# Performance work log

Hardware: AMD Instinct MI355X
Metric: run time of the kernel (lower is better)

The kernel has to match this reference:

```python
import jax, jax.numpy as jnp
import numpy as np

E = 8        # num_experts
K = 2        # num_experts_per_tok
H = 2048     # hidden_size
I = 1024     # intermediate_size (c_fc outputs 2*I for swiglu)
T = 4096     # tokens (batch*seq flattened)
STD = 0.02


def setup_inputs() -> dict:
    key = jax.random.key(0)
    k1, k2, k3, k4 = jax.random.split(key, 4)
    x = jax.random.normal(k1, (T, H), dtype=jnp.float32)
    router_w = jax.random.normal(k2, (E, H), dtype=jnp.float32) * STD   # nn.Linear(H->E, bias=False)
    w1 = jax.random.normal(k3, (E, 2 * I, H), dtype=jnp.float32) * STD  # c_fc.weight (E, out, in)
    w2 = jax.random.normal(k4, (E, H, I), dtype=jnp.float32) * STD      # c_proj.weight (E, out, in)
    return {"x": x, "router_w": router_w, "w1": w1, "w2": w2}


def reference(x, router_w, w1, w2):
    # Router: logits -> fp32 softmax -> top-k gates (no renorm), as in scattermoe-style MoE
    logits = x @ router_w.T                                   # (T, E)
    probs = jax.nn.softmax(logits.astype(jnp.float32), axis=-1)
    gates, expert_idx = jax.lax.top_k(probs, K)               # (T, K)

    # Grouped expert GEMMs, expressed densely over the small fixed expert axis.
    up = jnp.einsum('th,efh->etf', x, w1)                     # (E, T, 2I)  c_fc
    g = up[..., ::2]                                          # interleaved GLU gate
    u = up[..., 1::2]
    h = u * jax.nn.silu(g)                                    # swiglu, (E, T, I)
    y = jnp.einsum('eti,ehi->eth', h, w2)                     # (E, T, H)  c_proj

    # Scatter-combine: pick each token's top-k expert outputs, weight by gates.
    t = jnp.arange(T)[:, None]                                # (T, 1)
    sel = y[expert_idx, t]                                    # (T, K, H)
    out = jnp.sum(gates[..., None].astype(x.dtype) * sel, axis=1)  # (T, H)
    return out
```

## Files before the change

kernel.cpp:

```cpp
#include <hip/hip_runtime.h>
#include <hip/hip_bf16.h>
#include <stdint.h>

#define T_TOK 4096
#define H_DIM 2048
#define I_DIM 1024
#define E_NUM 8

using bf16x8  = __attribute__((ext_vector_type(8))) __bf16;
using f32x4   = __attribute__((ext_vector_type(4))) float;
using ushort8 = __attribute__((ext_vector_type(8))) unsigned short;

__device__ __forceinline__ unsigned short f2bf(float f) {
  unsigned int u = __float_as_uint(f);
  u += 0x7fffu + ((u >> 16) & 1u);
  return (unsigned short)(u >> 16);
}

__global__ void k_router(const float* __restrict__ x, const float* __restrict__ rw,
                         float* __restrict__ gates, int* __restrict__ idxs,
                         unsigned int* __restrict__ counts, unsigned short* __restrict__ xb) {
  int t = blockIdx.x;
  int lane = threadIdx.x;
  float acc[E_NUM];
#pragma unroll
  for (int e = 0; e < E_NUM; e++) acc[e] = 0.f;
  const float* xrow = x + (size_t)t * H_DIM;
  for (int h = lane; h < H_DIM; h += 64) {
    float xv = xrow[h];
    xb[(size_t)t * H_DIM + h] = f2bf(xv);
#pragma unroll
    for (int e = 0; e < E_NUM; e++) acc[e] += xv * rw[e * H_DIM + h];
  }
#pragma unroll
  for (int e = 0; e < E_NUM; e++) {
#pragma unroll
    for (int off = 32; off >= 1; off >>= 1) acc[e] += __shfl_xor(acc[e], off, 64);
  }
  if (lane == 0) {
    float mx = acc[0];
#pragma unroll
    for (int e = 1; e < E_NUM; e++) mx = fmaxf(mx, acc[e]);
    float p[E_NUM], s = 0.f;
#pragma unroll
    for (int e = 0; e < E_NUM; e++) { p[e] = __expf(acc[e] - mx); s += p[e]; }
    float inv = 1.f / s;
#pragma unroll
    for (int e = 0; e < E_NUM; e++) p[e] *= inv;
    int i1 = 0, i2 = 0; float m1 = -1.f, m2 = -1.f;
#pragma unroll
    for (int e = 0; e < E_NUM; e++) {
      float v = p[e];
      if (v > m1)      { m2 = m1; i2 = i1; m1 = v; i1 = e; }
      else if (v > m2) { m2 = v; i2 = e; }
    }
    gates[t * 2 + 0] = m1; gates[t * 2 + 1] = m2;
    idxs[t * 2 + 0] = i1;  idxs[t * 2 + 1] = i2;
    atomicAdd(&counts[i1], 1u);
    atomicAdd(&counts[i2], 1u);
  }
}

__global__ void k_offsets(const unsigned int* __restrict__ counts,
                          unsigned int* __restrict__ off, unsigned int* __restrict__ cursor) {
  if (threadIdx.x == 0 && blockIdx.x == 0) {
    unsigned int o = 0;
    for (int e = 0; e < E_NUM; e++) { off[e] = o; cursor[e] = o; o += counts[e]; }
  }
}

__global__ void k_scatter(const float* __restrict__ gates, const int* __restrict__ idxs,
                          unsigned int* __restrict__ cursor,
                          int* __restrict__ rowlist, float* __restrict__ rowgate) {
  int t = blockIdx.x * blockDim.x + threadIdx.x;
  if (t >= T_TOK) return;
#pragma unroll
  for (int k = 0; k < 2; k++) {
    int e = idxs[t * 2 + k];
    unsigned int pos = atomicAdd(&cursor[e], 1u);
    rowlist[pos] = t;
    rowgate[pos] = gates[t * 2 + k];
  }
}

__launch_bounds__(256, 2)
__global__ void k_gemm1(const unsigned short* __restrict__ xb, const float* __restrict__ w1,
                        const unsigned int* __restrict__ off, const unsigned int* __restrict__ counts,
                        const int* __restrict__ rowlist, unsigned short* __restrict__ hc) {
  int e = blockIdx.z;
  unsigned int cnt = counts[e];
  unsigned int rb = blockIdx.y;
  if (rb * 128u >= cnt) return;
  unsigned int o = off[e];
  int i0 = blockIdx.x * 64;

  __shared__ unsigned short a_lds[128 * 40];
  __shared__ unsigned short bg_lds[64 * 40];
  __shared__ unsigned short bu_lds[64 * 40];

  int tid = threadIdx.x;
  int lane = tid & 63;
  int wave = tid >> 6;
  int wr = wave >> 1;
  int wc = wave & 1;

  const float* w1e = w1 + (size_t)e * (2 * I_DIM) * H_DIM;

  f32x4 accg[4][2], accu[4][2];
#pragma unroll
  for (int m = 0; m < 4; m++)
#pragma unroll
    for (int n = 0; n < 2; n++) {
      accg[m][n] = f32x4{0.f, 0.f, 0.f, 0.f};
      accu[m][n] = f32x4{0.f, 0.f, 0.f, 0.f};
    }

  const unsigned short* asrc[2];
#pragma unroll
  for (int it = 0; it < 2; it++) {
    int flat = it * 256 + tid;
    int row = flat >> 2;
    unsigned int pos = rb * 128u + (unsigned int)row;
    unsigned int gp = o + (pos < cnt ? pos : cnt - 1u);
    int tok = rowlist[gp];
    asrc[it] = xb + (size_t)tok * H_DIM;
  }

  for (int k0 = 0; k0 < H_DIM; k0 += 32) {
    __syncthreads();
#pragma unroll
    for (int it = 0; it < 2; it++) {
      int flat = it * 256 + tid;
      int row = flat >> 2, q = flat & 3;
      ushort8 v = *reinterpret_cast<const ushort8*>(asrc[it] + k0 + q * 8);
      *reinterpret_cast<ushort8*>(&a_lds[row * 40 + q * 8]) = v;
    }
#pragma unroll
    for (int it = 0; it < 2; it++) {
      int flat = it * 256 + tid;
      int fl = flat >> 2, q = flat & 3;
      const float* src = w1e + (size_t)(2 * i0 + fl) * H_DIM + k0 + q * 8;
      float4 v0 = *reinterpret_cast<const float4*>(src);
      float4 v1 = *reinterpret_cast<const float4*>(src + 4);
      ushort8 b;
      b[0] = f2bf(v0.x); b[1] = f2bf(v0.y); b[2] = f2bf(v0.z); b[3] = f2bf(v0.w);
      b[4] = f2bf(v1.x); b[5] = f2bf(v1.y); b[6] = f2bf(v1.z); b[7] = f2bf(v1.w);
      unsigned short* dst = (fl & 1) ? bu_lds : bg_lds;
      *reinterpret_cast<ushort8*>(&dst[(fl >> 1) * 40 + q * 8]) = b;
    }
    __syncthreads();

    bf16x8 af[4], bgf[2], buf_[2];
#pragma unroll
    for (int m = 0; m < 4; m++) {
      int row = wr * 64 + m * 16 + (lane & 15);
      af[m] = *reinterpret_cast<const bf16x8*>(&a_lds[row * 40 + (lane >> 4) * 8]);
    }
#pragma unroll
    for (int n = 0; n < 2; n++) {
      int c = wc * 32 + n * 16 + (lane & 15);
      bgf[n]  = *reinterpret_cast<const bf16x8*>(&bg_lds[c * 40 + (lane >> 4) * 8]);
      buf_[n] = *reinterpret_cast<const bf16x8*>(&bu_lds[c * 40 + (lane >> 4) * 8]);
    }
#pragma unroll
    for (int m = 0; m < 4; m++)
#pragma unroll
      for (int n = 0; n < 2; n++) {
        accg[m][n] = __builtin_amdgcn_mfma_f32_16x16x32_bf16(af[m], bgf[n],  accg[m][n], 0, 0, 0);
        accu[m][n] = __builtin_amdgcn_mfma_f32_16x16x32_bf16(af[m], buf_[n], accu[m][n], 0, 0, 0);
      }
  }

#pragma unroll
  for (int m = 0; m < 4; m++)
#pragma unroll
    for (int n = 0; n < 2; n++)
#pragma unroll
      for (int r = 0; r < 4; r++) {
        unsigned int grow = rb * 128u + wr * 64 + m * 16 + (lane >> 4) * 4 + r;
        if (grow < cnt) {
          float g = accg[m][n][r], u = accu[m][n][r];
          float h = u * g / (1.f + __expf(-g));
          int ic = i0 + wc * 32 + n * 16 + (lane & 15);
          hc[(size_t)(o + grow) * I_DIM + ic] = f2bf(h);
        }
      }
}

__launch_bounds__(256, 2)
__global__ void k_gemm2(const unsigned short* __restrict__ hc, const float* __restrict__ w2,
                        const unsigned int* __restrict__ off, const unsigned int* __restrict__ counts,
                        const int* __restrict__ rowlist, const float* __restrict__ rowgate,
                        float* __restrict__ out) {
  int e = blockIdx.z;
  unsigned int cnt = counts[e];
  unsigned int rb = blockIdx.y;
  if (rb * 128u >= cnt) return;
  unsigned int o = off[e];
  int h0 = blockIdx.x * 128;

  __shared__ unsigned short a_lds[128 * 40];
  __shared__ unsigned short b_lds[128 * 40];

  int tid = threadIdx.x;
  int lane = tid & 63;
  int wave = tid >> 6;
  int wr = wave >> 1;
  int wc = wave & 1;

  const float* w2e = w2 + (size_t)e * H_DIM * I_DIM;

  f32x4 acc[4][4];
#pragma unroll
  for (int m = 0; m < 4; m++)
#pragma unroll
    for (int n = 0; n < 4; n++) acc[m][n] = f32x4{0.f, 0.f, 0.f, 0.f};

  const unsigned short* asrc[2];
#pragma unroll
  for (int it = 0; it < 2; it++) {
    int flat = it * 256 + tid;
    int row = flat >> 2;
    unsigned int pos = rb * 128u + (unsigned int)row;
    unsigned int gp = o + (pos < cnt ? pos : cnt - 1u);
    asrc[it] = hc + (size_t)gp * I_DIM;
  }

  for (int k0 = 0; k0 < I_DIM; k0 += 32) {
    __syncthreads();
#pragma unroll
    for (int it = 0; it < 2; it++) {
      int flat = it * 256 + tid;
      int row = flat >> 2, q = flat & 3;
      ushort8 v = *reinterpret_cast<const ushort8*>(asrc[it] + k0 + q * 8);
      *reinterpret_cast<ushort8*>(&a_lds[row * 40 + q * 8]) = v;
    }
#pragma unroll
    for (int it = 0; it < 2; it++) {
      int flat = it * 256 + tid;
      int fl = flat >> 2, q = flat & 3;
      const float* src = w2e + (size_t)(h0 + fl) * I_DIM + k0 + q * 8;
      float4 v0 = *reinterpret_cast<const float4*>(src);
      float4 v1 = *reinterpret_cast<const float4*>(src + 4);
      ushort8 b;
      b[0] = f2bf(v0.x); b[1] = f2bf(v0.y); b[2] = f2bf(v0.z); b[3] = f2bf(v0.w);
      b[4] = f2bf(v1.x); b[5] = f2bf(v1.y); b[6] = f2bf(v1.z); b[7] = f2bf(v1.w);
      *reinterpret_cast<ushort8*>(&b_lds[fl * 40 + q * 8]) = b;
    }
    __syncthreads();

    bf16x8 af[4], bf[4];
#pragma unroll
    for (int m = 0; m < 4; m++) {
      int row = wr * 64 + m * 16 + (lane & 15);
      af[m] = *reinterpret_cast<const bf16x8*>(&a_lds[row * 40 + (lane >> 4) * 8]);
    }
#pragma unroll
    for (int n = 0; n < 4; n++) {
      int c = wc * 64 + n * 16 + (lane & 15);
      bf[n] = *reinterpret_cast<const bf16x8*>(&b_lds[c * 40 + (lane >> 4) * 8]);
    }
#pragma unroll
    for (int m = 0; m < 4; m++)
#pragma unroll
      for (int n = 0; n < 4; n++)
        acc[m][n] = __builtin_amdgcn_mfma_f32_16x16x32_bf16(af[m], bf[n], acc[m][n], 0, 0, 0);
  }

#pragma unroll
  for (int m = 0; m < 4; m++)
#pragma unroll
    for (int r = 0; r < 4; r++) {
      unsigned int grow = rb * 128u + wr * 64 + m * 16 + (lane >> 4) * 4 + r;
      if (grow < cnt) {
        int tok = rowlist[o + grow];
        float gate = rowgate[o + grow];
        float* orow = out + (size_t)tok * H_DIM + h0 + wc * 64;
#pragma unroll
        for (int n = 0; n < 4; n++) {
          atomicAdd(&orow[n * 16 + (lane & 15)], gate * acc[m][n][r]);
        }
      }
    }
}

extern "C" void kernel_launch(void* const* d_in, const int* in_sizes, int n_in,
                              void* d_out, int out_size, void* d_ws, size_t ws_size,
                              hipStream_t stream) {
  const float* x  = (const float*)d_in[0];
  const float* rw = (const float*)d_in[1];
  const float* w1 = (const float*)d_in[2];
  const float* w2 = (const float*)d_in[3];
  float* out = (float*)d_out;

  char* ws = (char*)d_ws;
  unsigned int* counts = (unsigned int*)(ws + 0);
  unsigned int* cursor = (unsigned int*)(ws + 64);
  unsigned int* off    = (unsigned int*)(ws + 128);
  float* gates   = (float*)(ws + 4096);
  int*   idxs    = (int*)(ws + 4096 + 32768);
  int*   rowlist = (int*)(ws + 4096 + 65536);
  float* rowgate = (float*)(ws + 4096 + 98304);
  unsigned short* xb = (unsigned short*)(ws + (1u << 20));
  unsigned short* hc = (unsigned short*)(ws + (18u << 20));

  hipMemsetAsync(ws, 0, 256, stream);
  hipMemsetAsync(d_out, 0, (size_t)out_size * sizeof(float), stream);

  k_router<<<T_TOK, 64, 0, stream>>>(x, rw, gates, idxs, counts, xb);
  k_offsets<<<1, 64, 0, stream>>>(counts, off, cursor);
  k_scatter<<<T_TOK / 256, 256, 0, stream>>>(gates, idxs, cursor, rowlist, rowgate);
  k_gemm1<<<dim3(I_DIM / 64, T_TOK / 128, E_NUM), 256, 0, stream>>>(xb, w1, off, counts, rowlist, hc);
  k_gemm2<<<dim3(H_DIM / 128, T_TOK / 128, E_NUM), 256, 0, stream>>>(hc, w2, off, counts, rowlist, rowgate, out);
}
```

Baseline: 635.6 us.

## Pre-convert expert weights to bf16 and stream tiles via global_load_lds

Adds kernels that convert w1 (de-interleaved into separate gate and up planes) and w2 to bf16 once per call. The two GEMM kernels then load A and B tiles directly from global memory into LDS with global_load_lds, with no per-tile fp32 loads, conversion or register staging. The LDS row pitch drops from 40 to 32 elements, which may bring back bank conflicts, and launch bounds are raised to 3 blocks per CU. The cost is an extra pass over the fp32 weights plus a bf16 write and re-read, in exchange for halving weight traffic inside the GEMMs and removing repeated conversion work across row blocks.

```diff
diff --git a/kernel.cpp b/kernel.cpp
--- a/kernel.cpp
+++ b/kernel.cpp
@@ -15,6 +15,40 @@
   unsigned int u = __float_as_uint(f);
   u += 0x7fffu + ((u >> 16) & 1u);
   return (unsigned short)(u >> 16);
+}
+
+__device__ __forceinline__ void gload16(const unsigned short* g, unsigned short* l) {
+  __builtin_amdgcn_global_load_lds(
+      (const __attribute__((address_space(1))) unsigned int*)(g),
+      (__attribute__((address_space(3))) unsigned int*)(l), 16, 0, 0);
+}
+
+__global__ void k_cvt_w1(const float* __restrict__ w1, unsigned short* __restrict__ w1b) {
+  size_t idx = (size_t)blockIdx.x * 256 + threadIdx.x;
+  size_t d = idx * 8;
+  int h = (int)(d & (size_t)(H_DIM - 1));
+  size_t rem = d >> 11;
+  int i = (int)(rem & (size_t)(I_DIM - 1));
+  size_t rem2 = rem >> 10;
+  int gu = (int)(rem2 & 1);
+  int e = (int)(rem2 >> 1);
+  const float* src = w1 + (((size_t)e * 2 * I_DIM + 2 * i + gu) * H_DIM + h);
+  float4 v0 = *reinterpret_cast<const float4*>(src);
+  float4 v1 = *reinterpret_cast<const float4*>(src + 4);
+  ushort8 b;
+  b[0] = f2bf(v0.x); b[1] = f2bf(v0.y); b[2] = f2bf(v0.z); b[3] = f2bf(v0.w);
+  b[4] = f2bf(v1.x); b[5] = f2bf(v1.y); b[6] = f2bf(v1.z); b[7] = f2bf(v1.w);
+  *reinterpret_cast<ushort8*>(w1b + d) = b;
+}
+
+__global__ void k_cvt_w2(const float* __restrict__ w2, unsigned short* __restrict__ w2b) {
+  size_t d = ((size_t)blockIdx.x * 256 + threadIdx.x) * 8;
+  float4 v0 = *reinterpret_cast<const float4*>(w2 + d);
+  float4 v1 = *reinterpret_cast<const float4*>(w2 + d + 4);
+  ushort8 b;
+  b[0] = f2bf(v0.x); b[1] = f2bf(v0.y); b[2] = f2bf(v0.z); b[3] = f2bf(v0.w);
+  b[4] = f2bf(v1.x); b[5] = f2bf(v1.y); b[6] = f2bf(v1.z); b[7] = f2bf(v1.w);
+  *reinterpret_cast<ushort8*>(w2b + d) = b;
 }
 
 __global__ void k_router(const float* __restrict__ x, const float* __restrict__ rw,
@@ -83,8 +117,8 @@
   }
 }
 
-__launch_bounds__(256, 2)
-__global__ void k_gemm1(const unsigned short* __restrict__ xb, const float* __restrict__ w1,
+__launch_bounds__(256, 3)
+__global__ void k_gemm1(const unsigned short* __restrict__ xb, const unsigned short* __restrict__ w1b,
                         const unsigned int* __restrict__ off, const unsigned int* __restrict__ counts,
                         const int* __restrict__ rowlist, unsigned short* __restrict__ hc) {
   int e = blockIdx.z;
@@ -94,17 +128,31 @@
   unsigned int o = off[e];
   int i0 = blockIdx.x * 64;
 
-  __shared__ unsigned short a_lds[128 * 40];
-  __shared__ unsigned short bg_lds[64 * 40];
-  __shared__ unsigned short bu_lds[64 * 40];
-
-  int tid = threadIdx.x;
-  int lane = tid & 63;
-  int wave = tid >> 6;
-  int wr = wave >> 1;
-  int wc = wave & 1;
-
-  const float* w1e = w1 + (size_t)e * (2 * I_DIM) * H_DIM;
+  __shared__ unsigned short a_lds[128 * 32];
+  __shared__ unsigned short bg_lds[64 * 32];
+  __shared__ unsigned short bu_lds[64 * 32];
+
+  int tid = threadIdx.x, lane = tid & 63, wave = tid >> 6;
+  int wr = wave >> 1, wc = wave & 1;
+
+  const unsigned short* aptr[2];
+  unsigned short* alds[2];
+#pragma unroll
+  for (int it = 0; it < 2; it++) {
+    int flat = wave * 128 + it * 64 + lane;
+    int row = flat >> 2, colq = flat & 3;
+    unsigned int pos = rb * 128u + (unsigned int)row;
+    unsigned int gp = o + (pos < cnt ? pos : cnt - 1u);
+    int tok = rowlist[gp];
+    aptr[it] = xb + (size_t)tok * H_DIM + colq * 8;
+    alds[it] = &a_lds[(wave * 2 + it) * 512];
+  }
+  int flatB = wave * 64 + lane;
+  int brow = flatB >> 2, bcolq = flatB & 3;
+  const unsigned short* bptr_g = w1b + ((size_t)(e * 2 + 0) * I_DIM + i0 + brow) * H_DIM + bcolq * 8;
+  const unsigned short* bptr_u = w1b + ((size_t)(e * 2 + 1) * I_DIM + i0 + brow) * H_DIM + bcolq * 8;
+  unsigned short* blds_g = &bg_lds[wave * 512];
+  unsigned short* blds_u = &bu_lds[wave * 512];
 
   f32x4 accg[4][2], accu[4][2];
 #pragma unroll
@@ -115,52 +163,25 @@
       accu[m][n] = f32x4{0.f, 0.f, 0.f, 0.f};
     }
 
-  const unsigned short* asrc[2];
-#pragma unroll
-  for (int it = 0; it < 2; it++) {
-    int flat = it * 256 + tid;
-    int row = flat >> 2;
-    unsigned int pos = rb * 128u + (unsigned int)row;
-    unsigned int gp = o + (pos < cnt ? pos : cnt - 1u);
-    int tok = rowlist[gp];
-    asrc[it] = xb + (size_t)tok * H_DIM;
-  }
-
   for (int k0 = 0; k0 < H_DIM; k0 += 32) {
     __syncthreads();
-#pragma unroll
-    for (int it = 0; it < 2; it++) {
-      int flat = it * 256 + tid;
-      int row = flat >> 2, q = flat & 3;
-      ushort8 v = *reinterpret_cast<const ushort8*>(asrc[it] + k0 + q * 8);
-      *reinterpret_cast<ushort8*>(&a_lds[row * 40 + q * 8]) = v;
-    }
-#pragma unroll
-    for (int it = 0; it < 2; it++) {
-      int flat = it * 256 + tid;
-      int fl = flat >> 2, q = flat & 3;
-      const float* src = w1e + (size_t)(2 * i0 + fl) * H_DIM + k0 + q * 8;
-      float4 v0 = *reinterpret_cast<const float4*>(src);
-      float4 v1 = *reinterpret_cast<const float4*>(src + 4);
-      ushort8 b;
-      b[0] = f2bf(v0.x); b[1] = f2bf(v0.y); b[2] = f2bf(v0.z); b[3] = f2bf(v0.w);
-      b[4] = f2bf(v1.x); b[5] = f2bf(v1.y); b[6] = f2bf(v1.z); b[7] = f2bf(v1.w);
-      unsigned short* dst = (fl & 1) ? bu_lds : bg_lds;
-      *reinterpret_cast<ushort8*>(&dst[(fl >> 1) * 40 + q * 8]) = b;
-    }
+    gload16(aptr[0] + k0, alds[0]);
+    gload16(aptr[1] + k0, alds[1]);
+    gload16(bptr_g + k0, blds_g);
+    gload16(bptr_u + k0, blds_u);
     __syncthreads();
 
     bf16x8 af[4], bgf[2], buf_[2];
 #pragma unroll
     for (int m = 0; m < 4; m++) {
       int row = wr * 64 + m * 16 + (lane & 15);
-      af[m] = *reinterpret_cast<const bf16x8*>(&a_lds[row * 40 + (lane >> 4) * 8]);
+      af[m] = *reinterpret_cast<const bf16x8*>(&a_lds[row * 32 + (lane >> 4) * 8]);
     }
 #pragma unroll
     for (int n = 0; n < 2; n++) {
       int c = wc * 32 + n * 16 + (lane & 15);
-      bgf[n]  = *reinterpret_cast<const bf16x8*>(&bg_lds[c * 40 + (lane >> 4) * 8]);
-      buf_[n] = *reinterpret_cast<const bf16x8*>(&bu_lds[c * 40 + (lane >> 4) * 8]);
+      bgf[n]  = *reinterpret_cast<const bf16x8*>(&bg_lds[c * 32 + (lane >> 4) * 8]);
+      buf_[n] = *reinterpret_cast<const bf16x8*>(&bu_lds[c * 32 + (lane >> 4) * 8]);
     }
 #pragma unroll
     for (int m = 0; m < 4; m++)
@@ -187,8 +208,8 @@
       }
 }
 
-__launch_bounds__(256, 2)
-__global__ void k_gemm2(const unsigned short* __restrict__ hc, const float* __restrict__ w2,
+__launch_bounds__(256, 3)
+__global__ void k_gemm2(const unsigned short* __restrict__ hc, const unsigned short* __restrict__ w2b,
                         const unsigned int* __restrict__ off, const unsigned int* __restrict__ counts,
                         const int* __restrict__ rowlist, const float* __restrict__ rowgate,
                         float* __restrict__ out) {
@@ -199,66 +220,51 @@
   unsigned int o = off[e];
   int h0 = blockIdx.x * 128;
 
-  __shared__ unsigned short a_lds[128 * 40];
-  __shared__ unsigned short b_lds[128 * 40];
-
-  int tid = threadIdx.x;
-  int lane = tid & 63;
-  int wave = tid >> 6;
-  int wr = wave >> 1;
-  int wc = wave & 1;
-
-  const float* w2e = w2 + (size_t)e * H_DIM * I_DIM;
+  __shared__ unsigned short a_lds[128 * 32];
+  __shared__ unsigned short b_lds[128 * 32];
+
+  int tid = threadIdx.x, lane = tid & 63, wave = tid >> 6;
+  int wr = wave >> 1, wc = wave & 1;
+
+  const unsigned short* aptr[2];
+  const unsigned short* bptr[2];
+  unsigned short *alds[2], *blds[2];
+#pragma unroll
+  for (int it = 0; it < 2; it++) {
+    int flat = wave * 128 + it * 64 + lane;
+    int row = flat >> 2, colq = flat & 3;
+    unsigned int pos = rb * 128u + (unsigned int)row;
+    unsigned int posc = (pos < cnt ? pos : cnt - 1u);
+    aptr[it] = hc + (size_t)(o + posc) * I_DIM + colq * 8;
+    bptr[it] = w2b + ((size_t)e * H_DIM + h0 + row) * I_DIM + colq * 8;
+    alds[it] = &a_lds[(wave * 2 + it) * 512];
+    blds[it] = &b_lds[(wave * 2 + it) * 512];
+  }
 
   f32x4 acc[4][4];
 #pragma unroll
   for (int m = 0; m < 4; m++)
 #pragma unroll
     for (int n = 0; n < 4; n++) acc[m][n] = f32x4{0.f, 0.f, 0.f, 0.f};
-
-  const unsigned short* asrc[2];
-#pragma unroll
-  for (int it = 0; it < 2; it++) {
-    int flat = it * 256 + tid;
-    int row = flat >> 2;
-    unsigned int pos = rb * 128u + (unsigned int)row;
-    unsigned int gp = o + (pos < cnt ? pos : cnt - 1u);
-    asrc[it] = hc + (size_t)gp * I_DIM;
-  }
 
   for (int k0 = 0; k0 < I_DIM; k0 += 32) {
     __syncthreads();
-#pragma unroll
-    for (int it = 0; it < 2; it++) {
-      int flat = it * 256 + tid;
-      int row = flat >> 2, q = flat & 3;
-      ushort8 v = *reinterpret_cast<const ushort8*>(asrc[it] + k0 + q * 8);
-      *reinterpret_cast<ushort8*>(&a_lds[row * 40 + q * 8]) = v;
-    }
-#pragma unroll
-    for (int it = 0; it < 2; it++) {
-      int flat = it * 256 + tid;
-      int fl = flat >> 2, q = flat & 3;
-      const float* src = w2e + (size_t)(h0 + fl) * I_DIM + k0 + q * 8;
-      float4 v0 = *reinterpret_cast<const float4*>(src);
-      float4 v1 = *reinterpret_cast<const float4*>(src + 4);
-      ushort8 b;
-      b[0] = f2bf(v0.x); b[1] = f2bf(v0.y); b[2] = f2bf(v0.z); b[3] = f2bf(v0.w);
-      b[4] = f2bf(v1.x); b[5] = f2bf(v1.y); b[6] = f2bf(v1.z); b[7] = f2bf(v1.w);
-      *reinterpret_cast<ushort8*>(&b_lds[fl * 40 + q * 8]) = b;
-    }
+    gload16(aptr[0] + k0, alds[0]);
+    gload16(aptr[1] + k0, alds[1]);
+    gload16(bptr[0] + k0, blds[0]);
+    gload16(bptr[1] + k0, blds[1]);
     __syncthreads();
 
     bf16x8 af[4], bf[4];
 #pragma unroll
     for (int m = 0; m < 4; m++) {
       int row = wr * 64 + m * 16 + (lane & 15);
-      af[m] = *reinterpret_cast<const bf16x8*>(&a_lds[row * 40 + (lane >> 4) * 8]);
+      af[m] = *reinterpret_cast<const bf16x8*>(&a_lds[row * 32 + (lane >> 4) * 8]);
     }
 #pragma unroll
     for (int n = 0; n < 4; n++) {
       int c = wc * 64 + n * 16 + (lane & 15);
-      bf[n] = *reinterpret_cast<const bf16x8*>(&b_lds[c * 40 + (lane >> 4) * 8]);
+      bf[n] = *reinterpret_cast<const bf16x8*>(&b_lds[c * 32 + (lane >> 4) * 8]);
     }
 #pragma unroll
     for (int m = 0; m < 4; m++)
@@ -301,15 +307,20 @@
   int*   idxs    = (int*)(ws + 4096 + 32768);
   int*   rowlist = (int*)(ws + 4096 + 65536);
   float* rowgate = (float*)(ws + 4096 + 98304);
-  unsigned short* xb = (unsigned short*)(ws + (1u << 20));
-  unsigned short* hc = (unsigned short*)(ws + (18u << 20));
-
-  hipMemsetAsync(ws, 0, 256, stream);
+  unsigned short* xb  = (unsigned short*)(ws + (1ull << 20));
+  unsigned short* hc  = (unsigned short*)(ws + (17ull << 20));
+  unsigned short* w1b = (unsigned short*)(ws + (34ull << 20));
+  unsigned short* w2b = (unsigned short*)(ws + (100ull << 20));
+
+  hipMemsetAsync(ws, 0, 4096, stream);
   hipMemsetAsync(d_out, 0, (size_t)out_size * sizeof(float), stream);
+
+  k_cvt_w1<<<(E_NUM * 2 * I_DIM * (H_DIM / 8) + 255) / 256, 256, 0, stream>>>(w1, w1b);
+  k_cvt_w2<<<(E_NUM * H_DIM * (I_DIM / 8) + 255) / 256, 256, 0, stream>>>(w2, w2b);
 
   k_router<<<T_TOK, 64, 0, stream>>>(x, rw, gates, idxs, counts, xb);
   k_offsets<<<1, 64, 0, stream>>>(counts, off, cursor);
   k_scatter<<<T_TOK / 256, 256, 0, stream>>>(gates, idxs, cursor, rowlist, rowgate);
-  k_gemm1<<<dim3(I_DIM / 64, T_TOK / 128, E_NUM), 256, 0, stream>>>(xb, w1, off, counts, rowlist, hc);
-  k_gemm2<<<dim3(H_DIM / 128, T_TOK / 128, E_NUM), 256, 0, stream>>>(hc, w2, off, counts, rowlist, rowgate, out);
-}
+  k_gemm1<<<dim3(I_DIM / 64, T_TOK / 128, E_NUM), 256, 0, stream>>>(xb, w1b, off, counts, rowlist, hc);
+  k_gemm2<<<dim3(H_DIM / 128, T_TOK / 128, E_NUM), 256, 0, stream>>>(hc, w2b, off, counts, rowlist, rowgate, out);
+}
```

After: 635.9 us. Within noise of the previous version (+0.0%).
